# Kernel optimization log

Measured on AMD Instinct MI355X. Metric: run time of the kernel, lower is better.

## Reference

```python
import jax, jax.numpy as jnp
import numpy as np

D_IN, D_OUT, D_K, D_V, H = 768, 768, 64, 64, 12


def setup_inputs() -> dict:
    key = jax.random.key(0)
    ks = jax.random.split(key, 16)
    b, nq, nk = 4, 1024, 1024
    inp = {
        'queries': jax.random.normal(ks[0], (b, nq, D_IN), jnp.float32),
        'keys': jax.random.normal(ks[1], (b, nk, D_IN), jnp.float32),
        'values': jax.random.normal(ks[2], (b, nk, D_IN), jnp.float32),
        'loss_map': jax.random.normal(ks[3], (b, nk, H), jnp.float32),
        'attention_mask': jax.random.randint(ks[4], (b, H, nq, nk), 0, 2).astype(bool),
        'attention_weights': jax.random.uniform(ks[5], (b, H, nq, nk), jnp.float32),
        # learned params (stored as (in, out); math-equivalent to torch Linear)
        'Wq': jax.random.normal(ks[6], (D_IN, H * D_K), jnp.float32) * 0.02,
        'bq': jnp.zeros((H * D_K,), jnp.float32),
        'Wk': jax.random.normal(ks[7], (D_IN, H * D_K), jnp.float32) * 0.02,
        'bk': jnp.zeros((H * D_K,), jnp.float32),
        'Wv': jax.random.normal(ks[8], (D_IN, H * D_V), jnp.float32) * 0.02,
        'bv': jnp.zeros((H * D_V,), jnp.float32),
        'Wo': jax.random.normal(ks[9], (H * D_V, D_OUT), jnp.float32) * 0.02,
        'bo': jnp.zeros((D_OUT,), jnp.float32),
    }
    return inp


def reference(queries, keys, values, loss_map, attention_mask, attention_weights,
              Wq, bq, Wk, bk, Wv, bv, Wo, bo):
    b, nq, _ = queries.shape
    nk = keys.shape[1]
    # projections -> (b, h, n, d)
    q = (queries @ Wq + bq).reshape(b, nq, H, D_K).transpose(0, 2, 1, 3)
    k = (keys @ Wk + bk).reshape(b, nk, H, D_K).transpose(0, 2, 1, 3)
    v = (values @ Wv + bv).reshape(b, nk, H, D_V).transpose(0, 2, 1, 3)
    # scaled scores (b, h, nq, nk)
    att = jnp.einsum('bhqd,bhkd->bhqk', q, k) / np.sqrt(D_K).astype(np.float32)
    att = att * attention_weights
    att = jnp.where(attention_mask, -jnp.inf, att)
    # additive per-key, per-head bias: loss_map (b, nk, h) -> (b, h, 1, nk)
    w_g = loss_map.transpose(0, 2, 1)[:, :, None, :]
    w_mn = jax.nn.softmax(att + w_g, axis=-1)
    # dropout is identity in eval / p=0
    out = jnp.einsum('bhqk,bhkd->bhqd', w_mn, v)
    out = out.transpose(0, 2, 1, 3).reshape(b, nq, H * D_V)
    return out @ Wo + bo
```

## Files before the change

### kernel.cpp

```cpp
#include <hip/hip_runtime.h>
#include <hip/hip_bf16.h>
#include <hip/hip_fp16.h>
#include <cmath>

static constexpr int HN = 12;
static constexpr int DHEAD = 64;
static constexpr int DMODEL = 768;
static constexpr int NQ = 1024;
static constexpr int NB = 4;
static constexpr int NCH = 4;
static constexpr int MROWS = NB * NQ;
static constexpr size_t PER = (size_t)NB * HN * NQ * DHEAD;
static constexpr size_t WN  = (size_t)DMODEL * DMODEL;
static constexpr size_t CHROWS = (size_t)NB * HN * NQ;

typedef __attribute__((ext_vector_type(8))) short bf16x8;
typedef __attribute__((ext_vector_type(4))) float f32x4;

static __device__ __forceinline__ unsigned short f2bf(float f) {
    unsigned int u = __builtin_bit_cast(unsigned int, f);
    unsigned int r = (u + 0x7FFFu + ((u >> 16) & 1u)) >> 16;
    return (unsigned short)r;
}
static __device__ __forceinline__ unsigned pack2(float lo, float hi) {
    return (unsigned)f2bf(lo) | ((unsigned)f2bf(hi) << 16);
}
static __device__ __forceinline__ unsigned short f2h(float f) {
    return __half_as_ushort(__float2half(f));
}

typedef const __attribute__((address_space(1))) unsigned int gu32;
typedef __attribute__((address_space(3))) unsigned int lu32;
static __device__ __forceinline__ void gload16(const void* g, void* l) {
    __builtin_amdgcn_global_load_lds((gu32*)g, (lu32*)l, 16, 0, 0);
}

__global__ __launch_bounds__(256)
void cvt3(const float* __restrict__ a, const float* __restrict__ b, const float* __restrict__ c,
          unsigned short* __restrict__ oa, unsigned short* __restrict__ ob, unsigned short* __restrict__ oc)
{
    const int z = blockIdx.z;
    const float* s = z == 0 ? a : z == 1 ? b : c;
    unsigned short* d = z == 0 ? oa : z == 1 ? ob : oc;
    size_t i = ((size_t)blockIdx.x * 256 + threadIdx.x) * 4;
    float4 v = *(const float4*)&s[i];
    ushort4 u;
    u.x = f2bf(v.x); u.y = f2bf(v.y); u.z = f2bf(v.z); u.w = f2bf(v.w);
    *(ushort4*)&d[i] = u;
}

__global__ __launch_bounds__(256)
void wtrans(const float* __restrict__ w0, const float* __restrict__ w1,
            const float* __restrict__ w2, const float* __restrict__ w3,
            unsigned short* __restrict__ o0, unsigned short* __restrict__ o1,
            unsigned short* __restrict__ o2, unsigned short* __restrict__ o3)
{
    const int z = blockIdx.z;
    const float* in = z == 0 ? w0 : z == 1 ? w1 : z == 2 ? w2 : w3;
    unsigned short* out = z == 0 ? o0 : z == 1 ? o1 : z == 2 ? o2 : o3;
    __shared__ float t[64][65];
    const int tid = threadIdx.x;
    const int k0 = blockIdx.x * 64, n0 = blockIdx.y * 64;
    #pragma unroll
    for (int l = 0; l < 16; ++l) {
        int idx = l * 256 + tid, r = idx >> 6, cc = idx & 63;
        t[r][cc] = in[(size_t)(k0 + r) * DMODEL + n0 + cc];
    }
    __syncthreads();
    #pragma unroll
    for (int l = 0; l < 16; ++l) {
        int idx = l * 256 + tid, r = idx >> 6, cc = idx & 63;
        out[(size_t)(n0 + r) * DMODEL + k0 + cc] = f2bf(t[cc][r]);
    }
}

static __device__ __forceinline__
void gemm_body(const unsigned short* __restrict__ A, const unsigned short* __restrict__ Wt,
               const float* __restrict__ bias, void* __restrict__ C, int layout)
{
    constexpr int K = DMODEL;
    __shared__ unsigned short As[128 * 64];
    __shared__ unsigned short Bs[128 * 64];
    const int tid = threadIdx.x, w = tid >> 6, lane = tid & 63;
    const int c = lane & 15, g = lane >> 4;
    const int wr = w >> 1, wc = w & 1;
    const int bn = blockIdx.x * 128, bm = blockIdx.y * 128;

    f32x4 acc[4][4] = {};
    for (int k0 = 0; k0 < K; k0 += 64) {
        #pragma unroll
        for (int it = 0; it < 4; ++it) {
            int idx = it * 256 + tid, r = idx >> 3, blk = idx & 7;
            int so = (blk ^ (r & 7)) << 3;
            gload16(A  + (size_t)(bm + r) * K + k0 + so, &As[(it * 256 + w * 64) * 8]);
            gload16(Wt + (size_t)(bn + r) * K + k0 + so, &Bs[(it * 256 + w * 64) * 8]);
        }
        __syncthreads();
        #pragma unroll
        for (int kk = 0; kk < 2; ++kk) {
            bf16x8 a[4], b[4];
            #pragma unroll
            for (int mi = 0; mi < 4; ++mi) {
                int row = wr * 64 + mi * 16 + c;
                a[mi] = *(const bf16x8*)&As[row * 64 + ((((kk << 2) | g) ^ (row & 7)) << 3)];
            }
            #pragma unroll
            for (int ni = 0; ni < 4; ++ni) {
                int row = wc * 64 + ni * 16 + c;
                b[ni] = *(const bf16x8*)&Bs[row * 64 + ((((kk << 2) | g) ^ (row & 7)) << 3)];
            }
            #pragma unroll
            for (int mi = 0; mi < 4; ++mi)
                #pragma unroll
                for (int ni = 0; ni < 4; ++ni)
                    acc[mi][ni] = __builtin_amdgcn_mfma_f32_16x16x32_bf16(a[mi], b[ni], acc[mi][ni], 0, 0, 0);
        }
        __syncthreads();
    }

    #pragma unroll
    for (int ni = 0; ni < 4; ++ni) {
        int col = bn + wc * 64 + ni * 16 + c;
        float bvx = bias[col];
        int hh = col >> 6, d = col & 63;
        #pragma unroll
        for (int mi = 0; mi < 4; ++mi) {
            int m0 = bm + wr * 64 + mi * 16 + 4 * g;
            int bb = m0 >> 10, nn0 = m0 & (NQ - 1);
            if (layout == 0) {
                float* o = (float*)C;
                #pragma unroll
                for (int j = 0; j < 4; ++j)
                    o[(size_t)(m0 + j) * DMODEL + col] = acc[mi][ni][j] + bvx;
            } else if (layout == 1) {
                unsigned short* o = (unsigned short*)C;
                #pragma unroll
                for (int j = 0; j < 4; ++j)
                    o[(((size_t)bb * HN + hh) * NQ + nn0 + j) * DHEAD + d] =
                        f2bf(acc[mi][ni][j] + bvx);
            } else {
                unsigned short* o = (unsigned short*)C;
                ushort4 u;
                u.x = f2bf(acc[mi][ni][0] + bvx);
                u.y = f2bf(acc[mi][ni][1] + bvx);
                u.z = f2bf(acc[mi][ni][2] + bvx);
                u.w = f2bf(acc[mi][ni][3] + bvx);
                *(ushort4*)&o[(((size_t)bb * HN + hh) * DHEAD + d) * NQ + nn0] = u;
            }
        }
    }
}

__global__ __launch_bounds__(256)
void qkv_gemm(const unsigned short* __restrict__ qa, const unsigned short* __restrict__ ka,
              const unsigned short* __restrict__ va,
              const unsigned short* __restrict__ wq, const unsigned short* __restrict__ wk,
              const unsigned short* __restrict__ wv,
              const float* __restrict__ bq, const float* __restrict__ bk, const float* __restrict__ bv,
              unsigned short* __restrict__ qo, unsigned short* __restrict__ ko,
              unsigned short* __restrict__ vo)
{
    const int z = blockIdx.z;
    const unsigned short* A  = z == 0 ? qa : z == 1 ? ka : va;
    const unsigned short* Wt = z == 0 ? wq : z == 1 ? wk : wv;
    const float* bias        = z == 0 ? bq : z == 1 ? bk : bv;
    unsigned short* C        = z == 0 ? qo : z == 1 ? ko : vo;
    gemm_body(A, Wt, bias, C, z == 2 ? 2 : 1);
}

__global__ __launch_bounds__(256)
void o_gemm(const unsigned short* __restrict__ A, const unsigned short* __restrict__ Wt,
            const float* __restrict__ bias, float* __restrict__ C)
{
    gemm_body(A, Wt, bias, C, 0);
}

__global__ __launch_bounds__(256, 5)
void attn_part(const unsigned short* __restrict__ qws,
               const unsigned short* __restrict__ kws,
               const unsigned short* __restrict__ vtws,
               const float* __restrict__ aw, const int* __restrict__ mask,
               const float* __restrict__ lm,
               unsigned short* __restrict__ opart, float* __restrict__ mpart,
               float* __restrict__ lpart)
{
    const int qt = blockIdx.x, h = blockIdx.y;
    const int b = blockIdx.z >> 2, ch = blockIdx.z & 3;
    const int tid = threadIdx.x;
    const int w = tid >> 6, lane = tid & 63;
    const int c = lane & 15, g = lane >> 4;

    __shared__ unsigned short Ks[2][32 * 64];
    __shared__ unsigned short Vs[2][64 * 32];
    __shared__ float lms[256];

    const size_t bh = (size_t)b * HN + h;
    const unsigned short* qbase  = qws  + (bh * NQ + (size_t)qt * 64) * DHEAD;
    const unsigned short* kbase  = kws  + (bh * NQ + (size_t)ch * 256) * DHEAD;
    const unsigned short* vtbase = vtws + bh * DHEAD * NQ + ch * 256;

    auto stageKV = [&](int kt, int bufi) {
        {
            int r = tid >> 3, blk = tid & 7;
            int so = (blk ^ (r & 7)) << 3;
            gload16(kbase + (size_t)(kt * 32 + r) * DHEAD + so, &Ks[bufi][(w * 64) * 8]);
        }
        {
            int r = tid >> 2, blk = tid & 3;
            int so = ((blk ^ ((tid >> 4) & 3)) << 3);
            gload16(vtbase + (size_t)r * NQ + kt * 32 + so, &Vs[bufi][(w * 64) * 8]);
        }
    };

    const int qrow = w * 16 + c;
    const bf16x8 qf0 = *(const bf16x8*)&qbase[qrow * DHEAD + g * 8];
    const bf16x8 qf1 = *(const bf16x8*)&qbase[qrow * DHEAD + 32 + g * 8];

    const size_t awbase = (bh * NQ + (size_t)(qt * 64 + qrow)) * NQ + ch * 256;

    f32x4 O[4] = {{0,0,0,0},{0,0,0,0},{0,0,0,0},{0,0,0,0}};
    float mrun = -1e30f, lrun = 0.f;
    const int srcl = c + ((g & 1) << 5);
    const bool hiT = (g >> 1) != 0;
    const int vsw = (c >> 2);

    lms[tid] = lm[((size_t)b * NQ + ch * 256 + tid) * HN + h];
    stageKV(0, 0);
    __syncthreads();

    #pragma unroll
    for (int kt = 0; kt < 8; ++kt) {
        const int cur = kt & 1;
        if (kt < 7) stageKV(kt + 1, cur ^ 1);

        float4 aw4[2]; int4 mk4[2]; float4 lm4[2];
        #pragma unroll
        for (int nt = 0; nt < 2; ++nt) {
            size_t o = awbase + kt * 32 + nt * 16 + 4 * g;
            aw4[nt] = *(const float4*)&aw[o];
            mk4[nt] = *(const int4*)&mask[o];
            lm4[nt] = *(const float4*)&lms[kt * 32 + nt * 16 + 4 * g];
        }

        f32x4 s[2] = {{0,0,0,0},{0,0,0,0}};
        #pragma unroll
        for (int kk = 0; kk < 2; ++kk) {
            bf16x8 qf = kk ? qf1 : qf0;
            #pragma unroll
            for (int nt = 0; nt < 2; ++nt) {
                int krow = nt * 16 + c;
                bf16x8 kf = *(const bf16x8*)&Ks[cur][krow * 64 + ((((kk << 2) | g) ^ (c & 7)) << 3)];
                s[nt] = __builtin_amdgcn_mfma_f32_16x16x32_bf16(kf, qf, s[nt], 0, 0, 0);
            }
        }

        float p[2][4];
        float tmax = -INFINITY;
        #pragma unroll
        for (int nt = 0; nt < 2; ++nt) {
            const float* av = (const float*)&aw4[nt];
            const int*   mv = (const int*)&mk4[nt];
            const float* lv = (const float*)&lm4[nt];
            #pragma unroll
            for (int j = 0; j < 4; ++j) {
                float v = mv[j] ? -1e30f : fmaf(s[nt][j], 0.125f * av[j], lv[j]);
                p[nt][j] = v;
                tmax = fmaxf(tmax, v);
            }
        }
        tmax = fmaxf(tmax, __shfl_xor(tmax, 16));
        tmax = fmaxf(tmax, __shfl_xor(tmax, 32));

        float mn = fmaxf(mrun, tmax);
        float scal = __expf(mrun - mn);
        mrun = mn;
        float rs = 0.f;
        #pragma unroll
        for (int nt = 0; nt < 2; ++nt)
            #pragma unroll
            for (int j = 0; j < 4; ++j) {
                float e = __expf(p[nt][j] - mn);
                p[nt][j] = e;
                rs += e;
            }
        rs += __shfl_xor(rs, 16);
        rs += __shfl_xor(rs, 32);
        lrun = lrun * scal + rs;
        #pragma unroll
        for (int nd = 0; nd < 4; ++nd) O[nd] *= scal;

        int pk[2][2];
        #pragma unroll
        for (int nt = 0; nt < 2; ++nt) {
            pk[nt][0] = (int)pack2(p[nt][0], p[nt][1]);
            pk[nt][1] = (int)pack2(p[nt][2], p[nt][3]);
        }

        {
            int xa0 = __shfl(pk[0][0], srcl),      xb0 = __shfl(pk[1][0], srcl);
            int xa1 = __shfl(pk[0][1], srcl),      xb1 = __shfl(pk[1][1], srcl);
            int xa2 = __shfl(pk[0][0], srcl + 16), xb2 = __shfl(pk[1][0], srcl + 16);
            int xa3 = __shfl(pk[0][1], srcl + 16), xb3 = __shfl(pk[1][1], srcl + 16);
            int4 bi;
            bi.x = hiT ? xb0 : xa0;
            bi.y = hiT ? xb1 : xa1;
            bi.z = hiT ? xb2 : xa2;
            bi.w = hiT ? xb3 : xa3;
            bf16x8 pa = __builtin_bit_cast(bf16x8, bi);
            #pragma unroll
            for (int nd = 0; nd < 4; ++nd) {
                int vrow = nd * 16 + c;
                bf16x8 vf = *(const bf16x8*)&Vs[cur][vrow * 32 + ((g ^ vsw) << 3)];
                O[nd] = __builtin_amdgcn_mfma_f32_16x16x32_bf16(vf, pa, O[nd], 0, 0, 0);
            }
        }
        if (kt < 7) __syncthreads();
    }

    const size_t prow = ((size_t)(ch * NB + b) * HN + h) * NQ + qt * 64 + qrow;
    #pragma unroll
    for (int nd = 0; nd < 4; ++nd) {
        ushort4 u;
        u.x = f2h(O[nd][0]); u.y = f2h(O[nd][1]);
        u.z = f2h(O[nd][2]); u.w = f2h(O[nd][3]);
        *(ushort4*)&opart[prow * 64 + nd * 16 + 4 * g] = u;
    }
    if (g == 0) {
        mpart[prow] = mrun;
        lpart[prow] = lrun;
    }
}

__global__ __launch_bounds__(256)
void attn_combine(const unsigned short* __restrict__ opart, const float* __restrict__ mpart,
                  const float* __restrict__ lpart, unsigned short* __restrict__ out)
{
    const int qt = blockIdx.x, h = blockIdx.y, b = blockIdx.z;
    const int tid = threadIdx.x;
    const int q = qt * 64 + (tid >> 2);
    const int d0 = (tid & 3) * 16;
    const size_t row = ((size_t)b * HN + h) * NQ + q;

    float mv[4], lv[4];
    float M = -INFINITY;
    #pragma unroll
    for (int ci = 0; ci < 4; ++ci) {
        mv[ci] = mpart[ci * CHROWS + row];
        lv[ci] = lpart[ci * CHROWS + row];
        M = fmaxf(M, mv[ci]);
    }
    float L = 0.f;
    float wc[4];
    #pragma unroll
    for (int ci = 0; ci < 4; ++ci) {
        wc[ci] = __expf(mv[ci] - M);
        L += lv[ci] * wc[ci];
    }
    const float inv = 1.f / L;

    float o[16] = {};
    #pragma unroll
    for (int ci = 0; ci < 4; ++ci) {
        const unsigned short* src = opart + (ci * CHROWS + row) * 64 + d0;
        #pragma unroll
        for (int i = 0; i < 4; ++i) {
            ushort4 u = *(const ushort4*)&src[i * 4];
            o[i * 4 + 0] += wc[ci] * __half2float(__ushort_as_half(u.x));
            o[i * 4 + 1] += wc[ci] * __half2float(__ushort_as_half(u.y));
            o[i * 4 + 2] += wc[ci] * __half2float(__ushort_as_half(u.z));
            o[i * 4 + 3] += wc[ci] * __half2float(__ushort_as_half(u.w));
        }
    }
    const size_t ob = ((size_t)b * NQ + q) * DMODEL + h * DHEAD + d0;
    #pragma unroll
    for (int i = 0; i < 4; ++i) {
        ushort4 u;
        u.x = f2bf(o[i * 4 + 0] * inv);
        u.y = f2bf(o[i * 4 + 1] * inv);
        u.z = f2bf(o[i * 4 + 2] * inv);
        u.w = f2bf(o[i * 4 + 3] * inv);
        *(ushort4*)&out[ob + i * 4] = u;
    }
}

extern "C" void kernel_launch(void* const* d_in, const int* in_sizes, int n_in,
                              void* d_out, int out_size, void* d_ws, size_t ws_size,
                              hipStream_t stream)
{
    const float* queries = (const float*)d_in[0];
    const float* keys    = (const float*)d_in[1];
    const float* values  = (const float*)d_in[2];
    const float* lossmap = (const float*)d_in[3];
    const int*   mask    = (const int*)d_in[4];
    const float* aw      = (const float*)d_in[5];
    const float* Wq = (const float*)d_in[6];
    const float* bq = (const float*)d_in[7];
    const float* Wk = (const float*)d_in[8];
    const float* bk = (const float*)d_in[9];
    const float* Wv = (const float*)d_in[10];
    const float* bv = (const float*)d_in[11];
    const float* Wo = (const float*)d_in[12];
    const float* bo = (const float*)d_in[13];

    unsigned short* p = (unsigned short*)d_ws;
    unsigned short* qbf  = p; p += PER;
    unsigned short* kbf  = p; p += PER;
    unsigned short* vbf  = p; p += PER;
    unsigned short* qws  = p; p += PER;
    unsigned short* kws  = p; p += PER;
    unsigned short* vtws = p; p += PER;
    unsigned short* aobf = p; p += PER;
    unsigned short* wqt  = p; p += WN;
    unsigned short* wkt  = p; p += WN;
    unsigned short* wvt  = p; p += WN;
    unsigned short* wot  = p; p += WN;
    unsigned short* opart = p; p += (size_t)NCH * CHROWS * 64;
    float* fp = (float*)p;
    float* mpart = fp; fp += (size_t)NCH * CHROWS;
    float* lpart = fp; fp += (size_t)NCH * CHROWS;

    const int M = MROWS;
    cvt3<<<dim3((unsigned)(PER / 1024), 1, 3), 256, 0, stream>>>(queries, keys, values, qbf, kbf, vbf);
    wtrans<<<dim3(12, 12, 4), 256, 0, stream>>>(Wq, Wk, Wv, Wo, wqt, wkt, wvt, wot);
    qkv_gemm<<<dim3(DMODEL / 128, M / 128, 3), 256, 0, stream>>>(
        qbf, kbf, vbf, wqt, wkt, wvt, bq, bk, bv, qws, kws, vtws);
    attn_part<<<dim3(NQ / 64, HN, NB * NCH), 256, 0, stream>>>(
        qws, kws, vtws, aw, mask, lossmap, opart, mpart, lpart);
    attn_combine<<<dim3(NQ / 64, HN, NB), 256, 0, stream>>>(opart, mpart, lpart, aobf);
    o_gemm<<<dim3(DMODEL / 128, M / 128), 256, 0, stream>>>(aobf, wot, bo, (float*)d_out);
}
```

Before: 208.0 us.

## Precompute masked scaled weights as bf16 and stage them via LDS in attention

Adds a pre-pass that folds the mask, the 1/sqrt(d) scale and the attention weights into one bf16 tensor, using the sign bit to mark masked entries. The attention kernel then streams this compact tensor asynchronously into shared memory alongside K/V instead of loading fp32 weights and int mask per thread. This trades an extra full pass over the large weight/mask tensors for a lighter attention inner loop, and it reduces precision of the weights to bf16. The occupancy hint is also dropped.

After: 231.2 us. 1.11x slower.

```diff
diff --git a/kernel.cpp b/kernel.cpp
--- a/kernel.cpp
+++ b/kernel.cpp
@@ -13,6 +13,7 @@
 static constexpr size_t PER = (size_t)NB * HN * NQ * DHEAD;
 static constexpr size_t WN  = (size_t)DMODEL * DMODEL;
 static constexpr size_t CHROWS = (size_t)NB * HN * NQ;
+static constexpr size_t SCN = (size_t)NB * HN * NQ * NQ;
 
 typedef __attribute__((ext_vector_type(8))) short bf16x8;
 typedef __attribute__((ext_vector_type(4))) float f32x4;
@@ -28,11 +29,39 @@
 static __device__ __forceinline__ unsigned short f2h(float f) {
     return __half_as_ushort(__float2half(f));
 }
+static __device__ __forceinline__ float bf2f(unsigned short u) {
+    return __builtin_bit_cast(float, (unsigned)u << 16);
+}
 
 typedef const __attribute__((address_space(1))) unsigned int gu32;
 typedef __attribute__((address_space(3))) unsigned int lu32;
 static __device__ __forceinline__ void gload16(const void* g, void* l) {
     __builtin_amdgcn_global_load_lds((gu32*)g, (lu32*)l, 16, 0, 0);
+}
+
+__global__ __launch_bounds__(256)
+void fuse_scale(const float* __restrict__ aw, const int* __restrict__ mask,
+                unsigned short* __restrict__ scb)
+{
+    const size_t stride = (size_t)gridDim.x * 256 * 8;
+    size_t base = ((size_t)blockIdx.x * 256 + threadIdx.x) * 8;
+    for (; base < SCN; base += stride) {
+        float4 a0 = *(const float4*)&aw[base];
+        float4 a1 = *(const float4*)&aw[base + 4];
+        int4   m0 = *(const int4*)&mask[base];
+        int4   m1 = *(const int4*)&mask[base + 4];
+        ushort4 u0, u1;
+        u0.x = m0.x ? (unsigned short)0xBF80u : f2bf(0.125f * a0.x);
+        u0.y = m0.y ? (unsigned short)0xBF80u : f2bf(0.125f * a0.y);
+        u0.z = m0.z ? (unsigned short)0xBF80u : f2bf(0.125f * a0.z);
+        u0.w = m0.w ? (unsigned short)0xBF80u : f2bf(0.125f * a0.w);
+        u1.x = m1.x ? (unsigned short)0xBF80u : f2bf(0.125f * a1.x);
+        u1.y = m1.y ? (unsigned short)0xBF80u : f2bf(0.125f * a1.y);
+        u1.z = m1.z ? (unsigned short)0xBF80u : f2bf(0.125f * a1.z);
+        u1.w = m1.w ? (unsigned short)0xBF80u : f2bf(0.125f * a1.w);
+        *(ushort4*)&scb[base]     = u0;
+        *(ushort4*)&scb[base + 4] = u1;
+    }
 }
 
 __global__ __launch_bounds__(256)
@@ -175,11 +204,11 @@
     gemm_body(A, Wt, bias, C, 0);
 }
 
-__global__ __launch_bounds__(256, 5)
+__global__ __launch_bounds__(256)
 void attn_part(const unsigned short* __restrict__ qws,
                const unsigned short* __restrict__ kws,
                const unsigned short* __restrict__ vtws,
-               const float* __restrict__ aw, const int* __restrict__ mask,
+               const unsigned short* __restrict__ scb,
                const float* __restrict__ lm,
                unsigned short* __restrict__ opart, float* __restrict__ mpart,
                float* __restrict__ lpart)
@@ -192,55 +221,60 @@
 
     __shared__ unsigned short Ks[2][32 * 64];
     __shared__ unsigned short Vs[2][64 * 32];
+    __shared__ unsigned short scS[2][64 * 32];
     __shared__ float lms[256];
 
     const size_t bh = (size_t)b * HN + h;
     const unsigned short* qbase  = qws  + (bh * NQ + (size_t)qt * 64) * DHEAD;
     const unsigned short* kbase  = kws  + (bh * NQ + (size_t)ch * 256) * DHEAD;
     const unsigned short* vtbase = vtws + bh * DHEAD * NQ + ch * 256;
-
-    auto stageKV = [&](int kt, int bufi) {
+    const unsigned short* scbase = scb + (bh * NQ + (size_t)qt * 64) * NQ + ch * 256;
+
+    const int sq = tid >> 2;
+    const int sGs = (tid & 3) ^ (sq & 3);
+
+    auto stage = [&](int kt, int bufi) {
         {
             int r = tid >> 3, blk = tid & 7;
-            int so = (blk ^ (r & 7)) << 3;
-            gload16(kbase + (size_t)(kt * 32 + r) * DHEAD + so, &Ks[bufi][(w * 64) * 8]);
+            gload16(kbase + (size_t)(kt * 32 + r) * DHEAD + ((blk ^ (r & 7)) << 3),
+                    &Ks[bufi][w * 512]);
         }
         {
-            int r = tid >> 2, blk = tid & 3;
-            int so = ((blk ^ ((tid >> 4) & 3)) << 3);
-            gload16(vtbase + (size_t)r * NQ + kt * 32 + so, &Vs[bufi][(w * 64) * 8]);
+            int rv = tid >> 2, blkv = tid & 3;
+            gload16(vtbase + (size_t)rv * NQ + kt * 32 + ((blkv ^ ((tid >> 4) & 3)) << 3),
+                    &Vs[bufi][w * 512]);
+        }
+        {
+            gload16(scbase + (size_t)sq * NQ + kt * 32 + sGs * 8, &scS[bufi][w * 512]);
         }
     };
 
     const int qrow = w * 16 + c;
     const bf16x8 qf0 = *(const bf16x8*)&qbase[qrow * DHEAD + g * 8];
     const bf16x8 qf1 = *(const bf16x8*)&qbase[qrow * DHEAD + 32 + g * 8];
-
-    const size_t awbase = (bh * NQ + (size_t)(qt * 64 + qrow)) * NQ + ch * 256;
 
     f32x4 O[4] = {{0,0,0,0},{0,0,0,0},{0,0,0,0},{0,0,0,0}};
     float mrun = -1e30f, lrun = 0.f;
     const int srcl = c + ((g & 1) << 5);
     const bool hiT = (g >> 1) != 0;
     const int vsw = (c >> 2);
+    const int rpA = qrow * 32 + (((g >> 1) ^ (qrow & 3)) << 3) + ((g & 1) << 2);
+    const int rpB = qrow * 32 + (((2 + (g >> 1)) ^ (qrow & 3)) << 3) + ((g & 1) << 2);
 
     lms[tid] = lm[((size_t)b * NQ + ch * 256 + tid) * HN + h];
-    stageKV(0, 0);
+    stage(0, 0);
     __syncthreads();
 
     #pragma unroll
     for (int kt = 0; kt < 8; ++kt) {
         const int cur = kt & 1;
-        if (kt < 7) stageKV(kt + 1, cur ^ 1);
-
-        float4 aw4[2]; int4 mk4[2]; float4 lm4[2];
-        #pragma unroll
-        for (int nt = 0; nt < 2; ++nt) {
-            size_t o = awbase + kt * 32 + nt * 16 + 4 * g;
-            aw4[nt] = *(const float4*)&aw[o];
-            mk4[nt] = *(const int4*)&mask[o];
-            lm4[nt] = *(const float4*)&lms[kt * 32 + nt * 16 + 4 * g];
-        }
+        if (kt < 7) stage(kt + 1, cur ^ 1);
+
+        ushort4 sc4[2]; float4 lm4[2];
+        sc4[0] = *(const ushort4*)&scS[cur][rpA];
+        sc4[1] = *(const ushort4*)&scS[cur][rpB];
+        lm4[0] = *(const float4*)&lms[kt * 32 + 4 * g];
+        lm4[1] = *(const float4*)&lms[kt * 32 + 16 + 4 * g];
 
         f32x4 s[2] = {{0,0,0,0},{0,0,0,0}};
         #pragma unroll
@@ -258,12 +292,12 @@
         float tmax = -INFINITY;
         #pragma unroll
         for (int nt = 0; nt < 2; ++nt) {
-            const float* av = (const float*)&aw4[nt];
-            const int*   mv = (const int*)&mk4[nt];
+            const unsigned short* su = (const unsigned short*)&sc4[nt];
             const float* lv = (const float*)&lm4[nt];
             #pragma unroll
             for (int j = 0; j < 4; ++j) {
-                float v = mv[j] ? -1e30f : fmaf(s[nt][j], 0.125f * av[j], lv[j]);
+                unsigned short u = su[j];
+                float v = (u & 0x8000u) ? -1e30f : fmaf(s[nt][j], bf2f(u), lv[j]);
                 p[nt][j] = v;
                 tmax = fmaxf(tmax, v);
             }
@@ -341,18 +375,18 @@
     const int d0 = (tid & 3) * 16;
     const size_t row = ((size_t)b * HN + h) * NQ + q;
 
-    float mv[4], lv[4];
+    float mv[NCH], lv[NCH];
     float M = -INFINITY;
     #pragma unroll
-    for (int ci = 0; ci < 4; ++ci) {
+    for (int ci = 0; ci < NCH; ++ci) {
         mv[ci] = mpart[ci * CHROWS + row];
         lv[ci] = lpart[ci * CHROWS + row];
         M = fmaxf(M, mv[ci]);
     }
     float L = 0.f;
-    float wc[4];
-    #pragma unroll
-    for (int ci = 0; ci < 4; ++ci) {
+    float wc[NCH];
+    #pragma unroll
+    for (int ci = 0; ci < NCH; ++ci) {
         wc[ci] = __expf(mv[ci] - M);
         L += lv[ci] * wc[ci];
     }
@@ -360,7 +394,7 @@
 
     float o[16] = {};
     #pragma unroll
-    for (int ci = 0; ci < 4; ++ci) {
+    for (int ci = 0; ci < NCH; ++ci) {
         const unsigned short* src = opart + (ci * CHROWS + row) * 64 + d0;
         #pragma unroll
         for (int i = 0; i < 4; ++i) {
@@ -415,17 +449,19 @@
     unsigned short* wvt  = p; p += WN;
     unsigned short* wot  = p; p += WN;
     unsigned short* opart = p; p += (size_t)NCH * CHROWS * 64;
+    unsigned short* scb   = p; p += SCN;
     float* fp = (float*)p;
     float* mpart = fp; fp += (size_t)NCH * CHROWS;
     float* lpart = fp; fp += (size_t)NCH * CHROWS;
 
     const int M = MROWS;
+    fuse_scale<<<dim3(6144), 256, 0, stream>>>(aw, mask, scb);
     cvt3<<<dim3((unsigned)(PER / 1024), 1, 3), 256, 0, stream>>>(queries, keys, values, qbf, kbf, vbf);
     wtrans<<<dim3(12, 12, 4), 256, 0, stream>>>(Wq, Wk, Wv, Wo, wqt, wkt, wvt, wot);
     qkv_gemm<<<dim3(DMODEL / 128, M / 128, 3), 256, 0, stream>>>(
         qbf, kbf, vbf, wqt, wkt, wvt, bq, bk, bv, qws, kws, vtws);
     attn_part<<<dim3(NQ / 64, HN, NB * NCH), 256, 0, stream>>>(
-        qws, kws, vtws, aw, mask, lossmap, opart, mpart, lpart);
+        qws, kws, vtws, scb, lossmap, opart, mpart, lpart);
     attn_combine<<<dim3(NQ / 64, HN, NB), 256, 0, stream>>>(opart, mpart, lpart, aobf);
     o_gemm<<<dim3(DMODEL / 128, M / 128), 256, 0, stream>>>(aobf, wot, bo, (float*)d_out);
 }
```
